# Kernel tuning notes

Measured on AMD Instinct MI355X. Metric: run time of the kernel, lower is better.

The kernel has to match this reference:

```python
import jax, jax.numpy as jnp
import numpy as np

# --- batched state-vector quantum circuit sim: AngleEmbedding(RY) + BasicEntanglerLayers(RX + ring CNOT) ---

def _ry(state, theta, wire, n):
    # per-sample RY(theta) on `wire`; state: (B,) + (2,)*n complex
    ax = wire + 1
    c = jnp.cos(0.5 * theta).reshape((-1,) + (1,) * (n - 1)).astype(state.dtype)
    s = jnp.sin(0.5 * theta).reshape((-1,) + (1,) * (n - 1)).astype(state.dtype)
    s0 = jnp.take(state, 0, axis=ax)
    s1 = jnp.take(state, 1, axis=ax)
    return jnp.stack([c * s0 - s * s1, s * s0 + c * s1], axis=ax)

def _rx(state, theta, wire, n):
    # scalar RX(theta) on `wire` (shared weight across batch)
    ax = wire + 1
    c = jnp.cos(0.5 * theta).astype(state.dtype)
    s = (-1j * jnp.sin(0.5 * theta)).astype(state.dtype)
    s0 = jnp.take(state, 0, axis=ax)
    s1 = jnp.take(state, 1, axis=ax)
    return jnp.stack([c * s0 + s * s1, s * s0 + c * s1], axis=ax)

def _cnot(state, ctrl, tgt):
    ax_c = ctrl + 1
    s0 = jnp.take(state, 0, axis=ax_c)
    s1 = jnp.take(state, 1, axis=ax_c)
    ax_t = tgt + 1 if tgt < ctrl else tgt  # target axis index after removing ctrl axis
    s1 = jnp.flip(s1, axis=ax_t)
    return jnp.stack([s0, s1], axis=ax_c)

def _circuit(x_qin, qweights):
    # x_qin: (Bn, n) angles; qweights: (L, n)
    Bn, n = x_qin.shape
    state = jnp.zeros((Bn,) + (2,) * n, jnp.complex64)
    state = state.at[(slice(None),) + (0,) * n].set(1.0)
    for w in range(n):  # AngleEmbedding, rotation='Y'
        state = _ry(state, x_qin[:, w], w, n)
    for l in range(qweights.shape[0]):  # BasicEntanglerLayers
        for w in range(n):
            state = _rx(state, qweights[l, w], w, n)
        for w in range(n):
            state = _cnot(state, w, (w + 1) % n)
    probs = jnp.real(state * jnp.conj(state))
    outs = []
    for w in range(n):  # <Z_w> = P(bit_w=0) - P(bit_w=1)
        axes = tuple(a for a in range(1, n + 1) if a != w + 1)
        p = probs.sum(axis=axes)  # (Bn, 2)
        outs.append(p[:, 0] - p[:, 1])
    return jnp.stack(outs, axis=-1).astype(jnp.float32)


def setup_inputs() -> dict:
    key = jax.random.key(0)
    ks = jax.random.split(key, 9)
    B, N, H, NQ, L = 16, 1024, 256, 8, 2
    x = jax.random.normal(ks[0], (B, N, H), jnp.float32)
    norm_adj = jax.random.uniform(ks[1], (N, N), jnp.float32) / N
    Wg = jax.random.normal(ks[2], (H, H), jnp.float32) * 0.02
    bg = jax.random.normal(ks[3], (H,), jnp.float32) * 0.02
    Wpre = jax.random.normal(ks[4], (NQ, H), jnp.float32) * 0.05
    bpre = jax.random.normal(ks[5], (NQ,), jnp.float32) * 0.02
    qweights = jax.random.uniform(ks[6], (L, NQ), jnp.float32) * (2.0 * np.pi)
    Wpost = jax.random.normal(ks[7], (H, NQ), jnp.float32) * 0.1
    bpost = jax.random.normal(ks[8], (H,), jnp.float32) * 0.02
    return {"x": x, "norm_adj": norm_adj, "Wg": Wg, "bg": bg, "Wpre": Wpre,
            "bpre": bpre, "qweights": qweights, "Wpost": Wpost, "bpost": bpost}


def reference(x, norm_adj, Wg, bg, Wpre, bpre, qweights, Wpost, bpost):
    # GCN aggregation + GELU(Linear)  (dropout is identity in eval mode)
    x_agg = jnp.einsum('ij,bjh->bih', norm_adj, x)
    x_agg = jax.nn.gelu(x_agg @ Wg.T + bg, approximate=False)
    B, N, H = x_agg.shape
    x_flat = x_agg.reshape(B * N, H).astype(jnp.float32)
    x_qin = jnp.tanh(x_flat @ Wpre.T + bpre) * np.pi
    q_out = _circuit(x_qin, qweights)          # (B*N, n_qubits)
    out = (q_out @ Wpost.T + bpost).reshape(B, N, H)
    return out
```

## Files before the change

kernel.cpp:

```cpp
#include <hip/hip_runtime.h>
#include <math.h>

typedef __attribute__((ext_vector_type(8))) short bf16x8;
typedef _Float16 f16x8 __attribute__((ext_vector_type(8)));
typedef __attribute__((ext_vector_type(4))) float f32x4;

#define PI_F 3.14159265358979323846f

__device__ __forceinline__ unsigned short f2bf(float f) {
  unsigned int u = __float_as_uint(f);
  u += 0x7FFFu + ((u >> 16) & 1u);
  return (unsigned short)(u >> 16);
}

__device__ __forceinline__ float bf2f(unsigned short u) {
  return __uint_as_float(((unsigned int)u) << 16);
}

__device__ __forceinline__ void async_ld16(const unsigned short* g, unsigned short* l) {
  __builtin_amdgcn_global_load_lds(
      (const __attribute__((address_space(1))) void*)g,
      (__attribute__((address_space(3))) void*)l,
      16, 0, 0);
}

__device__ __forceinline__ float fast_erf(float x) {
  float a = fabsf(x);
  float t = 1.0f / fmaf(0.3275911f, a, 1.0f);
  float p = t * fmaf(t, fmaf(t, fmaf(t, fmaf(t, 1.061405429f, -1.453152027f),
                                     1.421413741f), -0.284496736f), 0.254829592f);
  float e = __expf(-a * a);
  float r = 1.0f - p * e;
  return copysignf(r, x);
}

__device__ __forceinline__ float fast_tanh(float a) {
  float e = __expf(2.0f * a);
  return 1.0f - 2.0f / (e + 1.0f);
}

template<int ML, int MR>
__device__ __forceinline__ void apply_rx(float re[4], float im[4], float c, float s) {
  float pr[4], pi[4];
  #pragma unroll
  for (int r = 0; r < 4; r++) {
    float vr = re[r ^ MR], vi = im[r ^ MR];
    if (ML) { vr = __shfl_xor(vr, ML, 64); vi = __shfl_xor(vi, ML, 64); }
    pr[r] = vr; pi[r] = vi;
  }
  #pragma unroll
  for (int r = 0; r < 4; r++) {
    re[r] = fmaf(c, re[r],  s * pi[r]);
    im[r] = fmaf(c, im[r], -s * pr[r]);
  }
}

__global__ __launch_bounds__(256)
void prep_kernel(const float* __restrict__ adj, unsigned short* __restrict__ adj_bf,
                 const float* __restrict__ Wg, unsigned short* __restrict__ Wg_bf,
                 const float* __restrict__ qw, unsigned short* __restrict__ Uri,
                 const float* __restrict__ Wpost, _Float16* __restrict__ Gt,
                 const float* __restrict__ x, unsigned short* __restrict__ xT) {
  __shared__ float smem[1056];
  int bid = blockIdx.x, t = threadIdx.x;
  if (bid < 1024) {
    int i = bid * 256 + t;
    float4 v = ((const float4*)adj)[i];
    ushort4 o; o.x = f2bf(v.x); o.y = f2bf(v.y); o.z = f2bf(v.z); o.w = f2bf(v.w);
    ((ushort4*)adj_bf)[i] = o;
  } else if (bid < 1088) {
    int i = (bid - 1024) * 256 + t;
    float4 v = ((const float4*)Wg)[i];
    ushort4 o; o.x = f2bf(v.x); o.y = f2bf(v.y); o.z = f2bf(v.z); o.w = f2bf(v.w);
    ((ushort4*)Wg_bf)[i] = o;
  } else if (bid < 1152) {
    if (t < 16) { smem[t] = cosf(0.5f * qw[t]); smem[16 + t] = sinf(0.5f * qw[t]); }
    __syncthreads();
    int wv = t >> 6, L = t & 63;
    int k = (bid - 1088) * 4 + wv;
    float re[4], im[4];
    #pragma unroll
    for (int r = 0; r < 4; r++) { re[r] = (r * 64 + L == k) ? 1.f : 0.f; im[r] = 0.f; }
    apply_rx<1, 0>(re, im, smem[0], smem[16]);
    apply_rx<2, 0>(re, im, smem[1], smem[17]);
    apply_rx<4, 0>(re, im, smem[2], smem[18]);
    apply_rx<8, 0>(re, im, smem[3], smem[19]);
    apply_rx<16, 0>(re, im, smem[4], smem[20]);
    apply_rx<32, 0>(re, im, smem[5], smem[21]);
    apply_rx<0, 1>(re, im, smem[6], smem[22]);
    apply_rx<0, 2>(re, im, smem[7], smem[23]);
    apply_rx<3, 0>(re, im, smem[8], smem[24]);
    apply_rx<6, 0>(re, im, smem[9], smem[25]);
    apply_rx<12, 0>(re, im, smem[10], smem[26]);
    apply_rx<24, 0>(re, im, smem[11], smem[27]);
    apply_rx<48, 0>(re, im, smem[12], smem[28]);
    apply_rx<32, 1>(re, im, smem[13], smem[29]);
    apply_rx<0, 3>(re, im, smem[14], smem[30]);
    apply_rx<3, 2>(re, im, smem[15], smem[31]);
    const int M[8] = {0xAB, 0xFD, 0xFA, 0xF5, 0xEA, 0xD5, 0xAA, 0x55};
    #pragma unroll
    for (int r = 0; r < 4; r++) {
      int n = 0;
      #pragma unroll
      for (int w = 0; w < 8; w++) {
        int bit = (__popc(L & (M[w] & 63)) ^ __popc((r << 6) & M[w])) & 1;
        n |= bit << w;
      }
      int row_re = ((n >> 4) << 5) + (n & 15);
      Uri[(size_t)row_re * 256 + k] = f2bf(re[r]);
      Uri[(size_t)(row_re + 16) * 256 + k] = f2bf(im[r]);
    }
  } else if (bid < 1168) {
    int tid = (bid - 1152) * 256 + t;
    int h = tid >> 4;
    int n0 = (tid & 15) << 4;
    float wv8[8];
    #pragma unroll
    for (int w = 0; w < 8; w++) wv8[w] = Wpost[h * 8 + w];
    #pragma unroll
    for (int j = 0; j < 16; j++) {
      int n = n0 + j;
      float sum = 0.f;
      #pragma unroll
      for (int w = 0; w < 8; w++) sum += ((n >> w) & 1) ? -wv8[w] : wv8[w];
      Gt[h * 256 + n] = (_Float16)sum;
    }
  } else {
    int tb = bid - 1168;
    int jt = tb & 31, ht = (tb >> 5) & 7, bb = tb >> 8;
    int tx = t & 31, ty = t >> 5;
    const float* xb = x + (size_t)bb * 1024 * 256;
    #pragma unroll
    for (int i = 0; i < 4; i++) {
      int j = jt * 32 + ty + i * 8;
      smem[(ty + i * 8) * 33 + tx] = xb[(size_t)j * 256 + ht * 32 + tx];
    }
    __syncthreads();
    unsigned short* xTb = xT + (size_t)bb * 256 * 1024;
    #pragma unroll
    for (int i = 0; i < 4; i++) {
      int h = ht * 32 + ty + i * 8;
      xTb[(size_t)h * 1024 + jt * 32 + tx] = f2bf(smem[tx * 33 + ty + i * 8]);
    }
  }
}

__global__ __launch_bounds__(256)
void gemm1_kernel(const unsigned short* __restrict__ A,
                  const unsigned short* __restrict__ Bt,
                  unsigned short* __restrict__ C,
                  int K, int tilesN, int ldC) {
  __shared__ unsigned short As[2 * 64 * 32];
  __shared__ unsigned short Bs[2 * 64 * 32];
  int rr  = blockIdx.x;
  int im  = rr / tilesN;
  int in_ = rr % tilesN;
  const unsigned short* Ab  = A  + (long long)im * 64 * K;
  const unsigned short* Btb = Bt + (long long)in_ * 64 * K;

  int t = threadIdx.x;
  int wv = t >> 6, lane = t & 63;
  int wm = wv >> 1, wn = wv & 1;
  int l15 = lane & 15, quad = lane >> 4;

  int srow = t >> 2;
  int skc  = (t & 3) ^ ((srow >> 1) & 3);
  long long sgo = (long long)srow * K + skc * 8;

  f32x4 acc[2][2] = {};

  for (int kk = 0; kk < K; kk += 64) {
    __syncthreads();
    #pragma unroll
    for (int kb = 0; kb < 2; kb++) {
      async_ld16(Ab + sgo + kk + kb * 32, &As[kb * 2048 + t * 8]);
      async_ld16(Btb + sgo + kk + kb * 32, &Bs[kb * 2048 + t * 8]);
    }
    __syncthreads();
    #pragma unroll
    for (int kb = 0; kb < 2; kb++) {
      bf16x8 af[2], bfr[2];
      #pragma unroll
      for (int mt = 0; mt < 2; mt++) {
        int row = wm * 32 + mt * 16 + l15;
        af[mt] = *(const bf16x8*)&As[kb * 2048 + row * 32 + ((quad ^ ((row >> 1) & 3)) * 8)];
      }
      #pragma unroll
      for (int nt = 0; nt < 2; nt++) {
        int row = wn * 32 + nt * 16 + l15;
        bfr[nt] = *(const bf16x8*)&Bs[kb * 2048 + row * 32 + ((quad ^ ((row >> 1) & 3)) * 8)];
      }
      #pragma unroll
      for (int mt = 0; mt < 2; mt++)
        #pragma unroll
        for (int nt = 0; nt < 2; nt++)
          acc[mt][nt] = __builtin_amdgcn_mfma_f32_16x16x32_bf16(af[mt], bfr[nt], acc[mt][nt], 0, 0, 0);
    }
  }

  int n0 = in_ * 64;
  #pragma unroll
  for (int mt = 0; mt < 2; mt++) {
    #pragma unroll
    for (int nt = 0; nt < 2; nt++) {
      int colg = n0 + wn * 32 + nt * 16 + l15;
      #pragma unroll
      for (int r = 0; r < 4; r++) {
        int rowg = im * 64 + wm * 32 + mt * 16 + quad * 4 + r;
        C[(size_t)rowg * ldC + colg] = f2bf(acc[mt][nt][r]);
      }
    }
  }
}

__global__ __launch_bounds__(512, 4)
void qfused_kernel(const unsigned short* __restrict__ xagg,
                   const unsigned short* __restrict__ Wg,
                   const float* __restrict__ bg,
                   const float* __restrict__ Wpre, const float* __restrict__ bpre,
                   const unsigned short* __restrict__ Uri,
                   const _Float16* __restrict__ Gt,
                   const float* __restrict__ bpost,
                   float* __restrict__ out) {
  __shared__ __align__(16) char smemraw[34816];
  unsigned short* gs  = (unsigned short*)smemraw;
  _Float16*       Ts  = (_Float16*)smemraw;
  unsigned short* P0s = (unsigned short*)(smemraw + 16384);
  float*          prt = (float*)(smemraw + 16384);
  float*          csw = (float*)(smemraw + 32768);

  int t = threadIdx.x;
  int wv = t >> 6, lane = t & 63;
  int l15 = lane & 15, quad = lane >> 4;

  const unsigned short* Ab = xagg + (size_t)blockIdx.x * 32 * 256;

  f32x4 acc[2][2] = {};
  {
    const unsigned short* Ap = Ab + (size_t)l15 * 256 + quad * 8;
    const unsigned short* Wp = Wg + (size_t)(wv * 32 + l15) * 256 + quad * 8;
    bf16x8 af[2][2], wf[2][2];
    #pragma unroll
    for (int sl = 0; sl < 2; sl++) {
      #pragma unroll
      for (int mt = 0; mt < 2; mt++) af[sl][mt] = *(const bf16x8*)(Ap + sl * 32 + mt * 4096);
      #pragma unroll
      for (int nt = 0; nt < 2; nt++) wf[sl][nt] = *(const bf16x8*)(Wp + sl * 32 + nt * 4096);
    }
    #pragma unroll
    for (int k8 = 0; k8 < 8; k8++) {
      int cur = k8 & 1;
      #pragma unroll
      for (int mt = 0; mt < 2; mt++)
        #pragma unroll
        for (int nt = 0; nt < 2; nt++)
          acc[mt][nt] = __builtin_amdgcn_mfma_f32_16x16x32_bf16(af[cur][mt], wf[cur][nt], acc[mt][nt], 0, 0, 0);
      if (k8 < 6) {
        #pragma unroll
        for (int mt = 0; mt < 2; mt++) af[cur][mt] = *(const bf16x8*)(Ap + (k8 + 2) * 32 + mt * 4096);
        #pragma unroll
        for (int nt = 0; nt < 2; nt++) wf[cur][nt] = *(const bf16x8*)(Wp + (k8 + 2) * 32 + nt * 4096);
      }
    }
  }
  #pragma unroll
  for (int mt = 0; mt < 2; mt++) {
    #pragma unroll
    for (int nt = 0; nt < 2; nt++) {
      int col = wv * 32 + nt * 16 + l15;
      float bgl = bg[col];
      int c = nt * 16 + l15, chunk = c >> 3, e = c & 7;
      #pragma unroll
      for (int r = 0; r < 4; r++) {
        int row = mt * 16 + quad * 4 + r;
        float v = acc[mt][nt][r] + bgl;
        v = 0.5f * v * (1.0f + fast_erf(v * 0.7071067811865475f));
        *(unsigned short*)((char*)gs + wv * 2048 + row * 64 +
                           ((chunk ^ ((row >> 1) & 3)) << 4) + e * 2) = f2bf(v);
      }
    }
  }
  __syncthreads();

  {
    const float* wrow = Wpre + (size_t)(l15 & 7) * 256 + wv * 32 + quad * 8;
    float4 wa = *(const float4*)wrow;
    float4 wb = *(const float4*)(wrow + 4);
    float v8[8] = {wa.x, wa.y, wa.z, wa.w, wb.x, wb.y, wb.z, wb.w};
    bf16x8 whi, wlo;
    #pragma unroll
    for (int j = 0; j < 8; j++) {
      unsigned short h = f2bf(v8[j]);
      whi[j] = (short)h;
      wlo[j] = (short)f2bf(v8[j] - bf2f(h));
    }
    const char* gp = (const char*)gs + wv * 2048;
    f32x4 aacc[2] = {};
    #pragma unroll
    for (int mt = 0; mt < 2; mt++) {
      int row = mt * 16 + l15;
      bf16x8 ga = *(const bf16x8*)(gp + row * 64 + ((quad ^ ((row >> 1) & 3)) << 4));
      aacc[mt] = __builtin_amdgcn_mfma_f32_16x16x32_bf16(ga, whi, aacc[mt], 0, 0, 0);
      aacc[mt] = __builtin_amdgcn_mfma_f32_16x16x32_bf16(ga, wlo, aacc[mt], 0, 0, 0);
    }
    if (l15 < 8) {
      #pragma unroll
      for (int mt = 0; mt < 2; mt++)
        #pragma unroll
        for (int r = 0; r < 4; r++)
          prt[wv * 256 + (mt * 16 + quad * 4 + r) * 8 + l15] = aacc[mt][r];
    }
  }
  __syncthreads();

  if (t < 256) {
    float s = 0.f;
    #pragma unroll
    for (int k = 0; k < 8; k++) s += prt[k * 256 + t];
    float th = (0.5f * PI_F) * fast_tanh(s + bpre[t & 7]);
    int row = t >> 3, w = t & 7;
    csw[row * 16 + w] = __cosf(th);
    csw[row * 16 + 8 + w] = __sinf(th);
  }
  __syncthreads();

  #pragma unroll
  for (int rr = 0; rr < 4; rr++) {
    int row = wv * 4 + rr;
    float4 c0 = *(const float4*)&csw[row * 16];
    float4 c1 = *(const float4*)&csw[row * 16 + 4];
    float4 s0 = *(const float4*)&csw[row * 16 + 8];
    float4 s1 = *(const float4*)&csw[row * 16 + 12];
    float cw[8] = {c0.x, c0.y, c0.z, c0.w, c1.x, c1.y, c1.z, c1.w};
    float sw[8] = {s0.x, s0.y, s0.z, s0.w, s1.x, s1.y, s1.z, s1.w};
    float pl = 1.f;
    #pragma unroll
    for (int b = 0; b < 6; b++) pl *= ((lane >> b) & 1) ? sw[b + 2] : cw[b + 2];
    ushort4 o;
    o.x = f2bf(pl * cw[0] * cw[1]);
    o.y = f2bf(pl * sw[0] * cw[1]);
    o.z = f2bf(pl * cw[0] * sw[1]);
    o.w = f2bf(pl * sw[0] * sw[1]);
    int jj = lane & 7;
    int cswz = (jj >> 1) ^ ((row >> 1) & 3);
    *(ushort4*)((char*)P0s + (lane >> 3) * 2048 + row * 64 + cswz * 16 + (jj & 1) * 8) = o;
  }
  __syncthreads();

  f32x4 acc1[2][4] = {};
  {
    const unsigned short* Up = Uri + (size_t)(wv * 64 + l15) * 256 + quad * 8;
    const char* Pp = (const char*)P0s + l15 * 64 + ((quad ^ ((l15 >> 1) & 3)) << 4);
    bf16x8 pa[2][2], ua[2][4];
    #pragma unroll
    for (int sl = 0; sl < 2; sl++) {
      #pragma unroll
      for (int mt = 0; mt < 2; mt++) pa[sl][mt] = *(const bf16x8*)(Pp + sl * 2048 + mt * 1024);
      #pragma unroll
      for (int nt = 0; nt < 4; nt++) ua[sl][nt] = *(const bf16x8*)(Up + sl * 32 + nt * 4096);
    }
    #pragma unroll
    for (int k8 = 0; k8 < 8; k8++) {
      int cur = k8 & 1;
      #pragma unroll
      for (int mt = 0; mt < 2; mt++)
        #pragma unroll
        for (int nt = 0; nt < 4; nt++)
          acc1[mt][nt] = __builtin_amdgcn_mfma_f32_16x16x32_bf16(pa[cur][mt], ua[cur][nt], acc1[mt][nt], 0, 0, 0);
      if (k8 < 6) {
        #pragma unroll
        for (int mt = 0; mt < 2; mt++) pa[cur][mt] = *(const bf16x8*)(Pp + (k8 + 2) * 2048 + mt * 1024);
        #pragma unroll
        for (int nt = 0; nt < 4; nt++) ua[cur][nt] = *(const bf16x8*)(Up + (k8 + 2) * 32 + nt * 4096);
      }
    }
  }

  #pragma unroll
  for (int mt = 0; mt < 2; mt++) {
    #pragma unroll
    for (int p = 0; p < 2; p++) {
      int c = p * 16 + l15, chunk = c >> 3, e = c & 7;
      #pragma unroll
      for (int r = 0; r < 4; r++) {
        int row = mt * 16 + quad * 4 + r;
        float tre = acc1[mt][2 * p][r], tim = acc1[mt][2 * p + 1][r];
        *(_Float16*)((char*)Ts + wv * 2048 + row * 64 +
                     ((chunk ^ ((row >> 1) & 3)) << 4) + e * 2)
            = (_Float16)(tre * tre + tim * tim);
      }
    }
  }
  __syncthreads();

  f32x4 acc2[2][2] = {};
  {
    const _Float16* Gp = Gt + (size_t)(wv * 32 + l15) * 256 + quad * 8;
    const char* Tp = (const char*)Ts + l15 * 64 + ((quad ^ ((l15 >> 1) & 3)) << 4);
    f16x8 tf[2][2], gf[2][2];
    #pragma unroll
    for (int sl = 0; sl < 2; sl++) {
      #pragma unroll
      for (int mt = 0; mt < 2; mt++) tf[sl][mt] = *(const f16x8*)(Tp + sl * 2048 + mt * 1024);
      #pragma unroll
      for (int nt = 0; nt < 2; nt++) gf[sl][nt] = *(const f16x8*)(Gp + sl * 32 + nt * 4096);
    }
    #pragma unroll
    for (int k8 = 0; k8 < 8; k8++) {
      int cur = k8 & 1;
      #pragma unroll
      for (int mt = 0; mt < 2; mt++)
        #pragma unroll
        for (int nt = 0; nt < 2; nt++)
          acc2[mt][nt] = __builtin_amdgcn_mfma_f32_16x16x32_f16(tf[cur][mt], gf[cur][nt], acc2[mt][nt], 0, 0, 0);
      if (k8 < 6) {
        #pragma unroll
        for (int mt = 0; mt < 2; mt++) tf[cur][mt] = *(const f16x8*)(Tp + (k8 + 2) * 2048 + mt * 1024);
        #pragma unroll
        for (int nt = 0; nt < 2; nt++) gf[cur][nt] = *(const f16x8*)(Gp + (k8 + 2) * 32 + nt * 4096);
      }
    }
  }

  #pragma unroll
  for (int mt = 0; mt < 2; mt++) {
    #pragma unroll
    for (int nt = 0; nt < 2; nt++) {
      int col = wv * 32 + nt * 16 + l15;
      float bp = bpost[col];
      #pragma unroll
      for (int r = 0; r < 4; r++) {
        int row = mt * 16 + quad * 4 + r;
        int s = blockIdx.x * 32 + row;
        int orow = (s & 15) * 1024 + (s >> 4);
        out[(size_t)orow * 256 + col] = acc2[mt][nt][r] + bp;
      }
    }
  }
}

extern "C" void kernel_launch(void* const* d_in, const int* in_sizes, int n_in,
                              void* d_out, int out_size, void* d_ws, size_t ws_size,
                              hipStream_t stream) {
  const float* x     = (const float*)d_in[0];
  const float* adj   = (const float*)d_in[1];
  const float* Wg    = (const float*)d_in[2];
  const float* bg    = (const float*)d_in[3];
  const float* Wpre  = (const float*)d_in[4];
  const float* bpre  = (const float*)d_in[5];
  const float* qw    = (const float*)d_in[6];
  const float* Wpost = (const float*)d_in[7];
  const float* bpost = (const float*)d_in[8];
  float* out = (float*)d_out;

  char* ws = (char*)d_ws;
  unsigned short* adj_bf  = (unsigned short*)(ws + 0);
  unsigned short* Wg_bf   = (unsigned short*)(ws + 2097152);
  unsigned short* xT_bf   = (unsigned short*)(ws + 2228224);
  unsigned short* xagg_bf = (unsigned short*)(ws + 10616832);
  unsigned short* Uri     = (unsigned short*)(ws + 19005440);
  _Float16*       Gt      = (_Float16*)(ws + 19267584);

  prep_kernel<<<5264, 256, 0, stream>>>(adj, adj_bf, Wg, Wg_bf, qw, Uri,
                                        Wpost, Gt, x, xT_bf);

  gemm1_kernel<<<1024, 256, 0, stream>>>(adj_bf, xT_bf, xagg_bf, 1024, 64, 4096);

  qfused_kernel<<<512, 512, 0, stream>>>(xagg_bf, Wg_bf, bg, Wpre, bpre, Uri, Gt, bpost, out);
}
```

Baseline: 142.8 us.

## Enlarge GEMM tiles, swizzle block order, and double qfused rows per block

The adjacency GEMM now uses 64x128 tiles with an XCD-aware block-index swizzle, halving the block count and reusing each A tile across more columns. The fused quantum kernel now processes 64 rows per block with 1024 threads. The xagg tile is staged once into LDS via async loads and shared by all waves, instead of each wave loading its rows from global memory. The aim is to cut redundant global loads and improve L2 locality, at the cost of more LDS per block (about 100KB), fewer blocks, and possibly lower occupancy.

Result: faster. 132.5 us (-7.2%).

```diff
diff --git a/kernel.cpp b/kernel.cpp
--- a/kernel.cpp
+++ b/kernel.cpp
@@ -151,59 +151,64 @@
                   unsigned short* __restrict__ C,
                   int K, int tilesN, int ldC) {
   __shared__ unsigned short As[2 * 64 * 32];
-  __shared__ unsigned short Bs[2 * 64 * 32];
-  int rr  = blockIdx.x;
-  int im  = rr / tilesN;
-  int in_ = rr % tilesN;
+  __shared__ unsigned short Bs[2 * 128 * 32];
+  int bid = blockIdx.x;
+  int swz = (bid & 7) * 64 + (bid >> 3);
+  int in_ = swz >> 4;
+  int im  = swz & 15;
   const unsigned short* Ab  = A  + (long long)im * 64 * K;
-  const unsigned short* Btb = Bt + (long long)in_ * 64 * K;
+  const unsigned short* Btb = Bt + (long long)in_ * 128 * K;
 
   int t = threadIdx.x;
   int wv = t >> 6, lane = t & 63;
   int wm = wv >> 1, wn = wv & 1;
   int l15 = lane & 15, quad = lane >> 4;
 
-  int srow = t >> 2;
-  int skc  = (t & 3) ^ ((srow >> 1) & 3);
-  long long sgo = (long long)srow * K + skc * 8;
-
-  f32x4 acc[2][2] = {};
+  f32x4 acc[2][4] = {};
 
   for (int kk = 0; kk < K; kk += 64) {
     __syncthreads();
     #pragma unroll
     for (int kb = 0; kb < 2; kb++) {
-      async_ld16(Ab + sgo + kk + kb * 32, &As[kb * 2048 + t * 8]);
-      async_ld16(Btb + sgo + kk + kb * 32, &Bs[kb * 2048 + t * 8]);
+      {
+        int r = t >> 2, c = (t & 3) ^ ((r >> 1) & 3);
+        async_ld16(Ab + (long long)r * K + kk + kb * 32 + c * 8, &As[kb * 2048 + t * 8]);
+      }
+      #pragma unroll
+      for (int q = 0; q < 2; q++) {
+        int sidx = q * 256 + t;
+        int r = sidx >> 2, c = (sidx & 3) ^ ((r >> 1) & 3);
+        async_ld16(Btb + (long long)r * K + kk + kb * 32 + c * 8, &Bs[kb * 4096 + sidx * 8]);
+      }
     }
     __syncthreads();
     #pragma unroll
     for (int kb = 0; kb < 2; kb++) {
-      bf16x8 af[2], bfr[2];
+      bf16x8 af[2], bfr[4];
       #pragma unroll
       for (int mt = 0; mt < 2; mt++) {
         int row = wm * 32 + mt * 16 + l15;
         af[mt] = *(const bf16x8*)&As[kb * 2048 + row * 32 + ((quad ^ ((row >> 1) & 3)) * 8)];
       }
       #pragma unroll
-      for (int nt = 0; nt < 2; nt++) {
-        int row = wn * 32 + nt * 16 + l15;
-        bfr[nt] = *(const bf16x8*)&Bs[kb * 2048 + row * 32 + ((quad ^ ((row >> 1) & 3)) * 8)];
+      for (int nt = 0; nt < 4; nt++) {
+        int row = wn * 64 + nt * 16 + l15;
+        bfr[nt] = *(const bf16x8*)&Bs[kb * 4096 + row * 32 + ((quad ^ ((row >> 1) & 3)) * 8)];
       }
       #pragma unroll
       for (int mt = 0; mt < 2; mt++)
         #pragma unroll
-        for (int nt = 0; nt < 2; nt++)
+        for (int nt = 0; nt < 4; nt++)
           acc[mt][nt] = __builtin_amdgcn_mfma_f32_16x16x32_bf16(af[mt], bfr[nt], acc[mt][nt], 0, 0, 0);
     }
   }
 
-  int n0 = in_ * 64;
+  int n0 = in_ * 128;
   #pragma unroll
   for (int mt = 0; mt < 2; mt++) {
     #pragma unroll
-    for (int nt = 0; nt < 2; nt++) {
-      int colg = n0 + wn * 32 + nt * 16 + l15;
+    for (int nt = 0; nt < 4; nt++) {
+      int colg = n0 + wn * 64 + nt * 16 + l15;
       #pragma unroll
       for (int r = 0; r < 4; r++) {
         int rowg = im * 64 + wm * 32 + mt * 16 + quad * 4 + r;
@@ -213,7 +218,7 @@
   }
 }
 
-__global__ __launch_bounds__(512, 4)
+__global__ __launch_bounds__(1024, 4)
 void qfused_kernel(const unsigned short* __restrict__ xagg,
                    const unsigned short* __restrict__ Wg,
                    const float* __restrict__ bg,
@@ -222,60 +227,60 @@
                    const _Float16* __restrict__ Gt,
                    const float* __restrict__ bpost,
                    float* __restrict__ out) {
-  __shared__ __align__(16) char smemraw[34816];
-  unsigned short* gs  = (unsigned short*)smemraw;
-  _Float16*       Ts  = (_Float16*)smemraw;
-  unsigned short* P0s = (unsigned short*)(smemraw + 16384);
-  float*          prt = (float*)(smemraw + 16384);
-  float*          csw = (float*)(smemraw + 32768);
+  __shared__ __align__(16) char smemraw[102400];
+  unsigned short* As  = (unsigned short*)smemraw;
+  unsigned short* gs  = (unsigned short*)(smemraw + 32768);
+  _Float16*       Ts  = (_Float16*)(smemraw + 32768);
+  unsigned short* P0s = (unsigned short*)(smemraw + 65536);
+  float*          prt = (float*)(smemraw + 65536);
+  float*          csw = (float*)(smemraw + 98304);
 
   int t = threadIdx.x;
   int wv = t >> 6, lane = t & 63;
   int l15 = lane & 15, quad = lane >> 4;
 
-  const unsigned short* Ab = xagg + (size_t)blockIdx.x * 32 * 256;
-
-  f32x4 acc[2][2] = {};
-  {
-    const unsigned short* Ap = Ab + (size_t)l15 * 256 + quad * 8;
-    const unsigned short* Wp = Wg + (size_t)(wv * 32 + l15) * 256 + quad * 8;
-    bf16x8 af[2][2], wf[2][2];
-    #pragma unroll
-    for (int sl = 0; sl < 2; sl++) {
-      #pragma unroll
-      for (int mt = 0; mt < 2; mt++) af[sl][mt] = *(const bf16x8*)(Ap + sl * 32 + mt * 4096);
-      #pragma unroll
-      for (int nt = 0; nt < 2; nt++) wf[sl][nt] = *(const bf16x8*)(Wp + sl * 32 + nt * 4096);
-    }
+  const unsigned short* Ab = xagg + (size_t)blockIdx.x * 64 * 256;
+
+  #pragma unroll
+  for (int q = 0; q < 2; q++) {
+    int sidx = q * 1024 + t;
+    int kb = sidx >> 8;
+    int r  = (sidx >> 2) & 63;
+    int c  = (sidx & 3) ^ ((r >> 1) & 3);
+    async_ld16(Ab + (size_t)r * 256 + kb * 32 + c * 8, &As[sidx * 8]);
+  }
+  __syncthreads();
+
+  f32x4 acc[4] = {};
+  {
+    const unsigned short* Wp = Wg + (size_t)(wv * 16 + l15) * 256 + quad * 8;
+    bf16x8 wf[2];
+    wf[0] = *(const bf16x8*)(Wp);
+    wf[1] = *(const bf16x8*)(Wp + 32);
     #pragma unroll
     for (int k8 = 0; k8 < 8; k8++) {
       int cur = k8 & 1;
       #pragma unroll
-      for (int mt = 0; mt < 2; mt++)
-        #pragma unroll
-        for (int nt = 0; nt < 2; nt++)
-          acc[mt][nt] = __builtin_amdgcn_mfma_f32_16x16x32_bf16(af[cur][mt], wf[cur][nt], acc[mt][nt], 0, 0, 0);
-      if (k8 < 6) {
-        #pragma unroll
-        for (int mt = 0; mt < 2; mt++) af[cur][mt] = *(const bf16x8*)(Ap + (k8 + 2) * 32 + mt * 4096);
-        #pragma unroll
-        for (int nt = 0; nt < 2; nt++) wf[cur][nt] = *(const bf16x8*)(Wp + (k8 + 2) * 32 + nt * 4096);
-      }
-    }
-  }
-  #pragma unroll
-  for (int mt = 0; mt < 2; mt++) {
-    #pragma unroll
-    for (int nt = 0; nt < 2; nt++) {
-      int col = wv * 32 + nt * 16 + l15;
-      float bgl = bg[col];
-      int c = nt * 16 + l15, chunk = c >> 3, e = c & 7;
+      for (int mt = 0; mt < 4; mt++) {
+        int row = mt * 16 + l15;
+        bf16x8 af = *(const bf16x8*)&As[k8 * 2048 + row * 32 + ((quad ^ ((row >> 1) & 3)) * 8)];
+        acc[mt] = __builtin_amdgcn_mfma_f32_16x16x32_bf16(af, wf[cur], acc[mt], 0, 0, 0);
+      }
+      if (k8 < 6) wf[cur] = *(const bf16x8*)(Wp + (k8 + 2) * 32);
+    }
+  }
+  {
+    int col = wv * 16 + l15;
+    float bgl = bg[col];
+    int kbc = col >> 5, chunk = (col >> 3) & 3, e = col & 7;
+    #pragma unroll
+    for (int mt = 0; mt < 4; mt++) {
       #pragma unroll
       for (int r = 0; r < 4; r++) {
         int row = mt * 16 + quad * 4 + r;
-        float v = acc[mt][nt][r] + bgl;
+        float v = acc[mt][r] + bgl;
         v = 0.5f * v * (1.0f + fast_erf(v * 0.7071067811865475f));
-        *(unsigned short*)((char*)gs + wv * 2048 + row * 64 +
+        *(unsigned short*)((char*)gs + kbc * 4096 + row * 64 +
                            ((chunk ^ ((row >> 1) & 3)) << 4) + e * 2) = f2bf(v);
       }
     }
@@ -283,7 +288,8 @@
   __syncthreads();
 
   {
-    const float* wrow = Wpre + (size_t)(l15 & 7) * 256 + wv * 32 + quad * 8;
+    int k8 = wv >> 1, mh = wv & 1;
+    const float* wrow = Wpre + (size_t)(l15 & 7) * 256 + k8 * 32 + quad * 8;
     float4 wa = *(const float4*)wrow;
     float4 wb = *(const float4*)(wrow + 4);
     float v8[8] = {wa.x, wa.y, wa.z, wa.w, wb.x, wb.y, wb.z, wb.w};
@@ -294,12 +300,12 @@
       whi[j] = (short)h;
       wlo[j] = (short)f2bf(v8[j] - bf2f(h));
     }
-    const char* gp = (const char*)gs + wv * 2048;
     f32x4 aacc[2] = {};
     #pragma unroll
     for (int mt = 0; mt < 2; mt++) {
-      int row = mt * 16 + l15;
-      bf16x8 ga = *(const bf16x8*)(gp + row * 64 + ((quad ^ ((row >> 1) & 3)) << 4));
+      int row = mh * 32 + mt * 16 + l15;
+      bf16x8 ga = *(const bf16x8*)((char*)gs + k8 * 4096 + row * 64 +
+                                   ((quad ^ ((row >> 1) & 3)) << 4));
       aacc[mt] = __builtin_amdgcn_mfma_f32_16x16x32_bf16(ga, whi, aacc[mt], 0, 0, 0);
       aacc[mt] = __builtin_amdgcn_mfma_f32_16x16x32_bf16(ga, wlo, aacc[mt], 0, 0, 0);
     }
@@ -308,15 +314,15 @@
       for (int mt = 0; mt < 2; mt++)
         #pragma unroll
         for (int r = 0; r < 4; r++)
-          prt[wv * 256 + (mt * 16 + quad * 4 + r) * 8 + l15] = aacc[mt][r];
-    }
-  }
-  __syncthreads();
-
-  if (t < 256) {
+          prt[k8 * 512 + (mh * 32 + mt * 16 + quad * 4 + r) * 8 + l15] = aacc[mt][r];
+    }
+  }
+  __syncthreads();
+
+  if (t < 512) {
     float s = 0.f;
     #pragma unroll
-    for (int k = 0; k < 8; k++) s += prt[k * 256 + t];
+    for (int k = 0; k < 8; k++) s += prt[k * 512 + t];
     float th = (0.5f * PI_F) * fast_tanh(s + bpre[t & 7]);
     int row = t >> 3, w = t & 7;
     csw[row * 16 + w] = __cosf(th);
@@ -343,49 +349,48 @@
     o.w = f2bf(pl * sw[0] * sw[1]);
     int jj = lane & 7;
     int cswz = (jj >> 1) ^ ((row >> 1) & 3);
-    *(ushort4*)((char*)P0s + (lane >> 3) * 2048 + row * 64 + cswz * 16 + (jj & 1) * 8) = o;
-  }
-  __syncthreads();
-
-  f32x4 acc1[2][4] = {};
-  {
-    const unsigned short* Up = Uri + (size_t)(wv * 64 + l15) * 256 + quad * 8;
-    const char* Pp = (const char*)P0s + l15 * 64 + ((quad ^ ((l15 >> 1) & 3)) << 4);
-    bf16x8 pa[2][2], ua[2][4];
-    #pragma unroll
-    for (int sl = 0; sl < 2; sl++) {
-      #pragma unroll
-      for (int mt = 0; mt < 2; mt++) pa[sl][mt] = *(const bf16x8*)(Pp + sl * 2048 + mt * 1024);
-      #pragma unroll
-      for (int nt = 0; nt < 4; nt++) ua[sl][nt] = *(const bf16x8*)(Up + sl * 32 + nt * 4096);
-    }
+    *(ushort4*)((char*)P0s + (lane >> 3) * 4096 + row * 64 + cswz * 16 + (jj & 1) * 8) = o;
+  }
+  __syncthreads();
+
+  f32x4 acc1[4][2] = {};
+  {
+    const unsigned short* Up = Uri + (size_t)(wv * 32 + l15) * 256 + quad * 8;
+    bf16x8 ua[2][2];
+    #pragma unroll
+    for (int sl = 0; sl < 2; sl++)
+      #pragma unroll
+      for (int nt = 0; nt < 2; nt++)
+        ua[sl][nt] = *(const bf16x8*)(Up + sl * 32 + nt * 4096);
     #pragma unroll
     for (int k8 = 0; k8 < 8; k8++) {
       int cur = k8 & 1;
       #pragma unroll
-      for (int mt = 0; mt < 2; mt++)
-        #pragma unroll
-        for (int nt = 0; nt < 4; nt++)
-          acc1[mt][nt] = __builtin_amdgcn_mfma_f32_16x16x32_bf16(pa[cur][mt], ua[cur][nt], acc1[mt][nt], 0, 0, 0);
+      for (int mt = 0; mt < 4; mt++) {
+        int row = mt * 16 + l15;
+        bf16x8 pa = *(const bf16x8*)((char*)P0s + k8 * 4096 + row * 64 +
+                                     ((quad ^ ((row >> 1) & 3)) << 4));
+        acc1[mt][0] = __builtin_amdgcn_mfma_f32_16x16x32_bf16(pa, ua[cur][0], acc1[mt][0], 0, 0, 0);
+        acc1[mt][1] = __builtin_amdgcn_mfma_f32_16x16x32_bf16(pa, ua[cur][1], acc1[mt][1], 0, 0, 0);
+      }
       if (k8 < 6) {
         #pragma unroll
-        for (int mt = 0; mt < 2; mt++) pa[cur][mt] = *(const bf16x8*)(Pp + (k8 + 2) * 2048 + mt * 1024);
-        #pragma unroll
-        for (int nt = 0; nt < 4; nt++) ua[cur][nt] = *(const bf16x8*)(Up + (k8 + 2) * 32 + nt * 4096);
-      }
-    }
-  }
-
-  #pragma unroll
-  for (int mt = 0; mt < 2; mt++) {
-    #pragma unroll
-    for (int p = 0; p < 2; p++) {
-      int c = p * 16 + l15, chunk = c >> 3, e = c & 7;
+        for (int nt = 0; nt < 2; nt++)
+          ua[cur][nt] = *(const bf16x8*)(Up + (k8 + 2) * 32 + nt * 4096);
+      }
+    }
+  }
+
+  {
+    int colT = wv * 16 + l15;
+    int kbc = colT >> 5, chunk = (colT >> 3) & 3, e = colT & 7;
+    #pragma unroll
+    for (int mt = 0; mt < 4; mt++) {
       #pragma unroll
       for (int r = 0; r < 4; r++) {
         int row = mt * 16 + quad * 4 + r;
-        float tre = acc1[mt][2 * p][r], tim = acc1[mt][2 * p + 1][r];
-        *(_Float16*)((char*)Ts + wv * 2048 + row * 64 +
+        float tre = acc1[mt][0][r], tim = acc1[mt][1][r];
+        *(_Float16*)((char*)Ts + kbc * 4096 + row * 64 +
                      ((chunk ^ ((row >> 1) & 3)) << 4) + e * 2)
             = (_Float16)(tre * tre + tim * tim);
       }
@@ -393,47 +398,37 @@
   }
   __syncthreads();
 
-  f32x4 acc2[2][2] = {};
-  {
-    const _Float16* Gp = Gt + (size_t)(wv * 32 + l15) * 256 + quad * 8;
-    const char* Tp = (const char*)Ts + l15 * 64 + ((quad ^ ((l15 >> 1) & 3)) << 4);
-    f16x8 tf[2][2], gf[2][2];
-    #pragma unroll
-    for (int sl = 0; sl < 2; sl++) {
-      #pragma unroll
-      for (int mt = 0; mt < 2; mt++) tf[sl][mt] = *(const f16x8*)(Tp + sl * 2048 + mt * 1024);
-      #pragma unroll
-      for (int nt = 0; nt < 2; nt++) gf[sl][nt] = *(const f16x8*)(Gp + sl * 32 + nt * 4096);
-    }
+  f32x4 acc2[4] = {};
+  {
+    const _Float16* Gp = Gt + (size_t)(wv * 16 + l15) * 256 + quad * 8;
+    f16x8 gf[2];
+    gf[0] = *(const f16x8*)(Gp);
+    gf[1] = *(const f16x8*)(Gp + 32);
     #pragma unroll
     for (int k8 = 0; k8 < 8; k8++) {
       int cur = k8 & 1;
       #pragma unroll
-      for (int mt = 0; mt < 2; mt++)
-        #pragma unroll
-        for (int nt = 0; nt < 2; nt++)
-          acc2[mt][nt] = __builtin_amdgcn_mfma_f32_16x16x32_f16(tf[cur][mt], gf[cur][nt], acc2[mt][nt], 0, 0, 0);
-      if (k8 < 6) {
-        #pragma unroll
-        for (int mt = 0; mt < 2; mt++) tf[cur][mt] = *(const f16x8*)(Tp + (k8 + 2) * 2048 + mt * 1024);
-        #pragma unroll
-        for (int nt = 0; nt < 2; nt++) gf[cur][nt] = *(const f16x8*)(Gp + (k8 + 2) * 32 + nt * 4096);
-      }
-    }
-  }
-
-  #pragma unroll
-  for (int mt = 0; mt < 2; mt++) {
-    #pragma unroll
-    for (int nt = 0; nt < 2; nt++) {
-      int col = wv * 32 + nt * 16 + l15;
-      float bp = bpost[col];
+      for (int mt = 0; mt < 4; mt++) {
+        int row = mt * 16 + l15;
+        f16x8 tf = *(const f16x8*)((char*)Ts + k8 * 4096 + row * 64 +
+                                   ((quad ^ ((row >> 1) & 3)) << 4));
+        acc2[mt] = __builtin_amdgcn_mfma_f32_16x16x32_f16(tf, gf[cur], acc2[mt], 0, 0, 0);
+      }
+      if (k8 < 6) gf[cur] = *(const f16x8*)(Gp + (k8 + 2) * 32);
+    }
+  }
+
+  {
+    int col = wv * 16 + l15;
+    float bp = bpost[col];
+    #pragma unroll
+    for (int mt = 0; mt < 4; mt++) {
       #pragma unroll
       for (int r = 0; r < 4; r++) {
         int row = mt * 16 + quad * 4 + r;
-        int s = blockIdx.x * 32 + row;
+        int s = blockIdx.x * 64 + row;
         int orow = (s & 15) * 1024 + (s >> 4);
-        out[(size_t)orow * 256 + col] = acc2[mt][nt][r] + bp;
+        out[(size_t)orow * 256 + col] = acc2[mt][r] + bp;
       }
     }
   }
@@ -464,7 +459,7 @@
   prep_kernel<<<5264, 256, 0, stream>>>(adj, adj_bf, Wg, Wg_bf, qw, Uri,
                                         Wpost, Gt, x, xT_bf);
 
-  gemm1_kernel<<<1024, 256, 0, stream>>>(adj_bf, xT_bf, xagg_bf, 1024, 64, 4096);
-
-  qfused_kernel<<<512, 512, 0, stream>>>(xagg_bf, Wg_bf, bg, Wpre, bpre, Uri, Gt, bpost, out);
-}
+  gemm1_kernel<<<512, 256, 0, stream>>>(adj_bf, xT_bf, xagg_bf, 1024, 32, 4096);
+
+  qfused_kernel<<<256, 1024, 0, stream>>>(xagg_bf, Wg_bf, bg, Wpre, bpre, Uri, Gt, bpost, out);
+}
```
